# Kernel tuning notes

Hardware: AMD Instinct MI355X
Metric: run time of the kernel (lower is better)

Reference implementation:

```python
import jax, jax.numpy as jnp
import numpy as np
import math

N_NODES = 50000
N_EDGES = 800000
IN_DIM = 128
OUT_DIM = 64
TIME_DIM = 128


def setup_inputs() -> dict:
    key = jax.random.key(0)
    ks = jax.random.split(key, 9)
    return {
        "node_feats": jax.random.normal(ks[0], (N_NODES, IN_DIM), dtype=jnp.float32),
        "time_diff": jax.random.uniform(ks[1], (N_EDGES,), dtype=jnp.float32),
        "src": jax.random.randint(ks[2], (N_EDGES,), 0, N_NODES, dtype=jnp.int32),
        "dst": jax.random.randint(ks[3], (N_EDGES,), 0, N_NODES, dtype=jnp.int32),
        "W": jax.random.normal(ks[4], (OUT_DIM, IN_DIM), dtype=jnp.float32) * 0.05,
        "Wv": jax.random.normal(ks[5], (OUT_DIM, IN_DIM), dtype=jnp.float32) * 0.05,
        "omega": jax.random.normal(ks[6], (TIME_DIM // 2,), dtype=jnp.float32),
        "Wt": jax.random.normal(ks[7], (OUT_DIM, TIME_DIM), dtype=jnp.float32) * 0.05,
        "a": jax.random.normal(ks[8], (3 * OUT_DIM,), dtype=jnp.float32) * 0.05,
    }


def reference(node_feats, time_diff, src, dst, W, Wv, omega, Wt, a):
    N = node_feats.shape[0]
    d = W.shape[0]  # out_dim
    time_dim = 2 * omega.shape[0]

    # gather + linear projections per edge
    h_src = node_feats[src] @ W.T          # [E, d]
    h_dst = node_feats[dst] @ W.T          # [E, d]
    v_src = node_feats[src] @ Wv.T         # [E, d]

    # temporal encoding: interleaved sin/cos of t * omega, scaled by sqrt(1/dim)
    ang = time_diff[:, None] * omega[None, :]                       # [E, dim/2]
    pe = jnp.stack([jnp.sin(ang), jnp.cos(ang)], axis=-1)
    pe = pe.reshape(ang.shape[0], time_dim) * jnp.float32(math.sqrt(1.0 / time_dim))
    t_emb = pe @ Wt.T                                               # [E, d]

    # attn_fc(concat([h_src, h_dst, t_emb])) == split dot products (same math, no big concat)
    e = h_src @ a[:d] + h_dst @ a[d:2 * d] + t_emb @ a[2 * d:]      # [E]
    e = jnp.where(e > 0, e, 0.2 * e)  # LeakyReLU(0.2)

    # edge_softmax: softmax over incoming edges of each destination node
    m = jax.ops.segment_max(e, dst, num_segments=N)
    ex = jnp.exp(e - m[dst])
    den = jax.ops.segment_sum(ex, dst, num_segments=N)
    alpha = ex / den[dst]  # dropout is identity in eval mode

    # weighted message scatter-sum aggregation
    msg = v_src * alpha[:, None]                                    # [E, d]
    return jax.ops.segment_sum(msg, dst, num_segments=N)            # [N, d]
```

## Files before the change

kernel.cpp:

```cpp
#include <hip/hip_runtime.h>
#include <hip/hip_bf16.h>
#include <hip/hip_fp16.h>
#include <math.h>

#define IN_DIM   128
#define OUT_DIM  64
#define THALF    64
#define PE_SCALE 0.08838834764831845f
#define TBL      2048

typedef __attribute__((ext_vector_type(8))) short  short8;
typedef __attribute__((ext_vector_type(4))) float  f32x4;

__device__ inline unsigned short bf16_rne(float x) {
    unsigned u = __float_as_uint(x);
    return (unsigned short)((u + 0x7FFFu + ((u >> 16) & 1u)) >> 16);
}

__global__ __launch_bounds__(256) void k_params_pack(
    const float* __restrict__ W, const float* __restrict__ Wt,
    const float* __restrict__ a, const float* __restrict__ Wv,
    float* __restrict__ atv, unsigned short* __restrict__ Bp)
{
    __shared__ float saW1[IN_DIM], saW2[IN_DIM];
    int k = threadIdx.x;
    if (k < IN_DIM) {
        float x1 = 0.f, x2 = 0.f, x3 = 0.f;
        for (int j = 0; j < OUT_DIM; ++j) {
            float wj = W[j * IN_DIM + k];
            x1 += a[j] * wj;
            x2 += a[OUT_DIM + j] * wj;
            x3 += a[2 * OUT_DIM + j] * Wt[j * IN_DIM + k];
        }
        saW1[k] = x1; saW2[k] = x2; atv[k] = x3;
    }
    __syncthreads();
    for (int i = threadIdx.x; i < 5 * 4 * 64 * 8; i += 256) {
        int j    = i & 7;
        int lane = (i >> 3) & 63;
        int k0i  = (i >> 9) & 3;
        int t    = i >> 11;
        int kk = k0i * 32 + (lane >> 4) * 8 + j;
        int n  = lane & 15;
        float val;
        if (t < 4)      val = Wv[(t * 16 + n) * IN_DIM + kk];
        else            val = (n == 0) ? saW1[kk] : (n == 1) ? saW2[kk] : 0.f;
        Bp[i] = bf16_rne(val);
    }
}

__global__ __launch_bounds__(256) void k_gtab(
    const float* __restrict__ omega,
    const float* __restrict__ atv,
    float* __restrict__ gtab,
    int* __restrict__ cnt, int N)
{
    int idx = blockIdx.x * 256 + threadIdx.x;
    if (idx <= TBL) {
        float t = (float)idx * (1.0f / TBL);
        float acc = 0.f;
#pragma unroll
        for (int i = 0; i < THALF; ++i) {
            float sp, cp;
            __sincosf(t * omega[i], &sp, &cp);
            acc += sp * atv[2 * i] + cp * atv[2 * i + 1];
        }
        gtab[idx] = acc;
    }
    for (int i = idx; i < N; i += gridDim.x * 256) cnt[i] = 0;
}

__global__ __launch_bounds__(256) void k_node_mfma(
    const float* __restrict__ feats,
    const unsigned short* __restrict__ Bp,
    unsigned short* __restrict__ vb,
    float* __restrict__ s1,
    float* __restrict__ s2,
    int N)
{
    int gwave = (blockIdx.x * 256 + threadIdx.x) >> 6;
    int lane  = threadIdx.x & 63;
    int ntiles = (N + 15) >> 4;
    if (gwave >= ntiles) return;
    int row = lane & 15, quad = lane >> 4;
    int nodeA = gwave * 16 + row;
    int nodeL = nodeA < N ? nodeA : N - 1;

    const float* arow = feats + (size_t)nodeL * IN_DIM + quad * 8;
    short8 afrag[4];
#pragma unroll
    for (int k0i = 0; k0i < 4; ++k0i) {
        float4 fa = *(const float4*)(arow + k0i * 32);
        float4 fb = *(const float4*)(arow + k0i * 32 + 4);
        union { unsigned u[4]; short8 s; } cv;
        cv.u[0] = (__float_as_uint(fa.x) >> 16) | (__float_as_uint(fa.y) & 0xFFFF0000u);
        cv.u[1] = (__float_as_uint(fa.z) >> 16) | (__float_as_uint(fa.w) & 0xFFFF0000u);
        cv.u[2] = (__float_as_uint(fb.x) >> 16) | (__float_as_uint(fb.y) & 0xFFFF0000u);
        cv.u[3] = (__float_as_uint(fb.z) >> 16) | (__float_as_uint(fb.w) & 0xFFFF0000u);
        afrag[k0i] = cv.s;
    }

    const short8* B8 = (const short8*)Bp;
    f32x4 acc[5];
#pragma unroll
    for (int t = 0; t < 5; ++t) acc[t] = (f32x4){0.f, 0.f, 0.f, 0.f};
#pragma unroll
    for (int t = 0; t < 5; ++t) {
#pragma unroll
        for (int k0i = 0; k0i < 4; ++k0i)
            acc[t] = __builtin_amdgcn_mfma_f32_16x16x32_bf16(
                afrag[k0i], B8[(t * 4 + k0i) * 64 + lane], acc[t], 0, 0, 0);
    }

    int col = lane & 15;
    int baseNode = gwave * 16 + quad * 4;
#pragma unroll
    for (int r = 0; r < 4; ++r) {
        int nd = baseNode + r;
        if (nd < N) {
            unsigned short* vr = vb + (size_t)nd * OUT_DIM + col;
#pragma unroll
            for (int t = 0; t < 4; ++t) vr[t * 16] = bf16_rne(acc[t][r]);
            if (col == 0)      s1[nd] = acc[4][r];
            else if (col == 1) s2[nd] = acc[4][r];
        }
    }
}

__global__ __launch_bounds__(256) void k_logits_rank(
    const float* __restrict__ tdiff,
    const int* __restrict__ src,
    const int* __restrict__ dst,
    const float* __restrict__ gtab,
    const float* __restrict__ s1,
    const float* __restrict__ s2,
    int* __restrict__ cnt,
    int* __restrict__ rank,
    unsigned* __restrict__ payw,
    int E)
{
    int e = blockIdx.x * blockDim.x + threadIdx.x;
    if (e >= E) return;
    int s = src[e], d = dst[e];
    int rk = atomicAdd(cnt + d, 1);
    float a1 = s1[s];
    float a2 = s2[d];
    float t = tdiff[e];

    float x = t * (float)TBL;
    int i0 = (int)x;
    i0 = i0 < 0 ? 0 : (i0 > TBL - 1 ? TBL - 1 : i0);
    float fr = x - (float)i0;
    float g0 = gtab[i0], g1 = gtab[i0 + 1];
    float ev = a1 + a2 + PE_SCALE * (g0 + fr * (g1 - g0));
    ev = ev > 0.f ? ev : 0.2f * ev;

    rank[e] = rk;
    payw[e] = ((unsigned)s << 16) | (unsigned)__half_as_ushort(__float2half(ev));
}

__global__ __launch_bounds__(256) void k_scan1(const int* __restrict__ cnt,
                                               int* __restrict__ offs,
                                               int* __restrict__ bsum, int N)
{
    __shared__ int lds[256];
    int b = blockIdx.x, t = threadIdx.x;
    int base = b * 1024 + t * 4;
    int v0 = (base + 0 < N) ? cnt[base + 0] : 0;
    int v1 = (base + 1 < N) ? cnt[base + 1] : 0;
    int v2 = (base + 2 < N) ? cnt[base + 2] : 0;
    int v3 = (base + 3 < N) ? cnt[base + 3] : 0;
    int s = v0 + v1 + v2 + v3;
    lds[t] = s;
    __syncthreads();
    for (int off = 1; off < 256; off <<= 1) {
        int tmp = (t >= off) ? lds[t - off] : 0;
        __syncthreads();
        lds[t] += tmp;
        __syncthreads();
    }
    int ex = lds[t] - s;
    if (base + 0 < N) offs[base + 0] = ex;
    ex += v0;
    if (base + 1 < N) offs[base + 1] = ex;
    ex += v1;
    if (base + 2 < N) offs[base + 2] = ex;
    ex += v2;
    if (base + 3 < N) offs[base + 3] = ex;
    if (t == 255) bsum[b] = lds[255];
}

__global__ __launch_bounds__(256) void k_scan3(int* __restrict__ offs,
                                               const int* __restrict__ bsum,
                                               int N, int E)
{
    int i = blockIdx.x * 256 + threadIdx.x;
    if (i < N) {
        int c = i >> 10;
        int p = 0;
        for (int j = 0; j < c; ++j) p += bsum[j];
        offs[i] += p;
    }
    if (i == 0) offs[N] = E;
}

__global__ __launch_bounds__(256) void k_scatter(
    const int* __restrict__ dst,
    const int* __restrict__ rank,
    const unsigned* __restrict__ payw,
    const int* __restrict__ offs,
    unsigned* __restrict__ payload,
    int E)
{
    int e = blockIdx.x * blockDim.x + threadIdx.x;
    if (e >= E) return;
    payload[offs[dst[e]] + rank[e]] = payw[e];
}

__global__ __launch_bounds__(256) void k_aggregate(
    const int* __restrict__ offs,
    const unsigned* __restrict__ payload,
    const unsigned short* __restrict__ vb,
    float* __restrict__ out,
    int N)
{
    int wid  = (blockIdx.x * blockDim.x + threadIdx.x) >> 6;
    int lane = threadIdx.x & 63;
    if (wid >= N) return;
    int beg = offs[wid];
    int deg = offs[wid + 1] - beg;
    int g8 = lane >> 3, r = lane & 7;

    float acc[8];
#pragma unroll
    for (int i = 0; i < 8; ++i) acc[i] = 0.f;
    float den = 0.f;

    for (int base = 0; base < deg; base += 64) {
        int cl = deg - base; if (cl > 64) cl = 64;
        bool valid = lane < cl;
        unsigned pl = valid ? payload[beg + base + lane] : 0u;
        float ex = valid ? __expf(__half2float(__ushort_as_half((unsigned short)(pl & 0xFFFFu)))) : 0.f;
        int   sv = valid ? (int)(pl >> 16) : 0;

        float sum = ex;
#pragma unroll
        for (int off = 32; off; off >>= 1) sum += __shfl_xor(sum, off, 64);
        den += sum;

        int rounds = (cl + 15) >> 4;
        for (int j = 0; j < rounds; ++j) {
            int i0 = j * 16 + g8;
            int i1 = i0 + 8;
            float e0 = __shfl(ex, i0, 64);
            int   s0 = __shfl(sv, i0, 64);
            float e1 = __shfl(ex, i1, 64);
            int   s1v = __shfl(sv, i1, 64);
            uint4 w0 = *((const uint4*)(vb + (size_t)s0 * OUT_DIM) + r);
            uint4 w1 = *((const uint4*)(vb + (size_t)s1v * OUT_DIM) + r);
            acc[0] += e0 * __uint_as_float(w0.x << 16)        + e1 * __uint_as_float(w1.x << 16);
            acc[1] += e0 * __uint_as_float(w0.x & 0xFFFF0000u) + e1 * __uint_as_float(w1.x & 0xFFFF0000u);
            acc[2] += e0 * __uint_as_float(w0.y << 16)        + e1 * __uint_as_float(w1.y << 16);
            acc[3] += e0 * __uint_as_float(w0.y & 0xFFFF0000u) + e1 * __uint_as_float(w1.y & 0xFFFF0000u);
            acc[4] += e0 * __uint_as_float(w0.z << 16)        + e1 * __uint_as_float(w1.z << 16);
            acc[5] += e0 * __uint_as_float(w0.z & 0xFFFF0000u) + e1 * __uint_as_float(w1.z & 0xFFFF0000u);
            acc[6] += e0 * __uint_as_float(w0.w << 16)        + e1 * __uint_as_float(w1.w << 16);
            acc[7] += e0 * __uint_as_float(w0.w & 0xFFFF0000u) + e1 * __uint_as_float(w1.w & 0xFFFF0000u);
        }
    }

#pragma unroll
    for (int i = 0; i < 8; ++i) {
        acc[i] += __shfl_xor(acc[i], 8, 64);
        acc[i] += __shfl_xor(acc[i], 16, 64);
        acc[i] += __shfl_xor(acc[i], 32, 64);
    }

    if (g8 == 0) {
        float inv = (deg > 0) ? 1.f / den : 0.f;
        float* o = out + (size_t)wid * OUT_DIM + r * 8;
        *(float4*)(o)     = make_float4(acc[0] * inv, acc[1] * inv, acc[2] * inv, acc[3] * inv);
        *(float4*)(o + 4) = make_float4(acc[4] * inv, acc[5] * inv, acc[6] * inv, acc[7] * inv);
    }
}

extern "C" void kernel_launch(void* const* d_in, const int* in_sizes, int n_in,
                              void* d_out, int out_size, void* d_ws, size_t ws_size,
                              hipStream_t stream) {
    const float* feats = (const float*)d_in[0];
    const float* tdiff = (const float*)d_in[1];
    const int*   src   = (const int*)d_in[2];
    const int*   dst   = (const int*)d_in[3];
    const float* W     = (const float*)d_in[4];
    const float* Wv    = (const float*)d_in[5];
    const float* omega = (const float*)d_in[6];
    const float* Wt    = (const float*)d_in[7];
    const float* a     = (const float*)d_in[8];
    float* out = (float*)d_out;

    int N = in_sizes[0] / IN_DIM;
    int E = in_sizes[1];

    int offs_elems = ((N + 1 + 3) / 4) * 4;
    float* ws      = (float*)d_ws;
    unsigned short* vb = (unsigned short*)ws;
    float* s1      = ws + (size_t)N * 32;
    float* s2      = s1 + N;
    int*   rank    = (int*)(s2 + N);
    unsigned* payw = (unsigned*)(rank + E);
    unsigned* payload = payw + E;
    int*   cnt     = (int*)(payload + E);
    int*   offs    = cnt + N;
    int*   bsum    = offs + offs_elems;
    float* atv     = (float*)(bsum + 64);
    float* gtab    = atv + IN_DIM;
    unsigned short* Bp = (unsigned short*)(gtab + TBL + 1);

    int nb = (N + 1023) / 1024;
    int ntiles = (N + 15) / 16;

    k_params_pack<<<1, 256, 0, stream>>>(W, Wt, a, Wv, atv, Bp);
    k_gtab<<<64, 256, 0, stream>>>(omega, atv, gtab, cnt, N);
    k_node_mfma<<<(ntiles * 64 + 255) / 256, 256, 0, stream>>>(feats, Bp, vb, s1, s2, N);
    k_logits_rank<<<(E + 255) / 256, 256, 0, stream>>>(tdiff, src, dst, gtab, s1, s2, cnt, rank, payw, E);
    k_scan1<<<nb, 256, 0, stream>>>(cnt, offs, bsum, N);
    k_scan3<<<(N + 255) / 256, 256, 0, stream>>>(offs, bsum, N, E);
    k_scatter<<<(E + 255) / 256, 256, 0, stream>>>(dst, rank, payw, offs, payload, E);
    long long tot = (long long)N * OUT_DIM;
    k_aggregate<<<(int)((tot + 255) / 256), 256, 0, stream>>>(offs, payload, vb, out, N);
}
```

Measured before the change: 194.3 us.

## Fuse edge logits, counting scan and scatter into one cooperative kernel

Merges the edge logit/rank, two scan passes and the scatter into a single cooperative-groups kernel on 256 blocks, with grid syncs between phases. Per-edge rank, destination and payload stay in registers (up to 16 edges per thread), so the rank and payw global arrays and their round trip through memory go away. The cnt zeroing moves from k_gtab into the fused kernel. In exchange, the edge phase runs on only 65536 threads with serialised loops and the grid-wide syncs cost something. Correctness depends on E <= 16 x 65536 and on the cooperative launch succeeding.

```diff
diff --git a/kernel.cpp b/kernel.cpp
--- a/kernel.cpp
+++ b/kernel.cpp
@@ -1,13 +1,18 @@
 #include <hip/hip_runtime.h>
 #include <hip/hip_bf16.h>
 #include <hip/hip_fp16.h>
+#include <hip/hip_cooperative_groups.h>
 #include <math.h>
+
+namespace cg = cooperative_groups;
 
 #define IN_DIM   128
 #define OUT_DIM  64
 #define THALF    64
 #define PE_SCALE 0.08838834764831845f
 #define TBL      2048
+#define CB       256
+#define MAXE     16
 
 typedef __attribute__((ext_vector_type(8))) short  short8;
 typedef __attribute__((ext_vector_type(4))) float  f32x4;
@@ -52,22 +57,19 @@
 __global__ __launch_bounds__(256) void k_gtab(
     const float* __restrict__ omega,
     const float* __restrict__ atv,
-    float* __restrict__ gtab,
-    int* __restrict__ cnt, int N)
+    float* __restrict__ gtab)
 {
     int idx = blockIdx.x * 256 + threadIdx.x;
-    if (idx <= TBL) {
-        float t = (float)idx * (1.0f / TBL);
-        float acc = 0.f;
-#pragma unroll
-        for (int i = 0; i < THALF; ++i) {
-            float sp, cp;
-            __sincosf(t * omega[i], &sp, &cp);
-            acc += sp * atv[2 * i] + cp * atv[2 * i + 1];
-        }
-        gtab[idx] = acc;
-    }
-    for (int i = idx; i < N; i += gridDim.x * 256) cnt[i] = 0;
+    if (idx > TBL) return;
+    float t = (float)idx * (1.0f / TBL);
+    float acc = 0.f;
+#pragma unroll
+    for (int i = 0; i < THALF; ++i) {
+        float sp, cp;
+        __sincosf(t * omega[i], &sp, &cp);
+        acc += sp * atv[2 * i] + cp * atv[2 * i + 1];
+    }
+    gtab[idx] = acc;
 }
 
 __global__ __launch_bounds__(256) void k_node_mfma(
@@ -127,7 +129,7 @@
     }
 }
 
-__global__ __launch_bounds__(256) void k_logits_rank(
+__global__ __launch_bounds__(256) void k_edge_coop(
     const float* __restrict__ tdiff,
     const int* __restrict__ src,
     const int* __restrict__ dst,
@@ -135,86 +137,83 @@
     const float* __restrict__ s1,
     const float* __restrict__ s2,
     int* __restrict__ cnt,
-    int* __restrict__ rank,
-    unsigned* __restrict__ payw,
-    int E)
-{
-    int e = blockIdx.x * blockDim.x + threadIdx.x;
-    if (e >= E) return;
-    int s = src[e], d = dst[e];
-    int rk = atomicAdd(cnt + d, 1);
-    float a1 = s1[s];
-    float a2 = s2[d];
-    float t = tdiff[e];
-
-    float x = t * (float)TBL;
-    int i0 = (int)x;
-    i0 = i0 < 0 ? 0 : (i0 > TBL - 1 ? TBL - 1 : i0);
-    float fr = x - (float)i0;
-    float g0 = gtab[i0], g1 = gtab[i0 + 1];
-    float ev = a1 + a2 + PE_SCALE * (g0 + fr * (g1 - g0));
-    ev = ev > 0.f ? ev : 0.2f * ev;
-
-    rank[e] = rk;
-    payw[e] = ((unsigned)s << 16) | (unsigned)__half_as_ushort(__float2half(ev));
-}
-
-__global__ __launch_bounds__(256) void k_scan1(const int* __restrict__ cnt,
-                                               int* __restrict__ offs,
-                                               int* __restrict__ bsum, int N)
-{
+    int* __restrict__ offs,
+    int* __restrict__ bsum,
+    unsigned* __restrict__ payload,
+    int N, int E)
+{
+    cg::grid_group grid = cg::this_grid();
+    int tid = blockIdx.x * 256 + threadIdx.x;
+    const int T = CB * 256;
+
+    for (int i = tid; i < N; i += T) cnt[i] = 0;
+    grid.sync();
+
+    int      ed[MAXE];
+    int      rk[MAXE];
+    unsigned pw[MAXE];
+    int ne = 0;
+    for (int e = tid; e < E; e += T) {
+        int s = src[e], d = dst[e];
+        int r = atomicAdd(cnt + d, 1);
+        float a1 = s1[s];
+        float a2 = s2[d];
+        float t = tdiff[e];
+        float x = t * (float)TBL;
+        int i0 = (int)x;
+        i0 = i0 < 0 ? 0 : (i0 > TBL - 1 ? TBL - 1 : i0);
+        float fr = x - (float)i0;
+        float g0 = gtab[i0], g1 = gtab[i0 + 1];
+        float ev = a1 + a2 + PE_SCALE * (g0 + fr * (g1 - g0));
+        ev = ev > 0.f ? ev : 0.2f * ev;
+        ed[ne] = d;
+        rk[ne] = r;
+        pw[ne] = ((unsigned)s << 16) | (unsigned)__half_as_ushort(__float2half(ev));
+        ++ne;
+    }
+    grid.sync();
+
+    int nb = (N + 1023) >> 10;
     __shared__ int lds[256];
-    int b = blockIdx.x, t = threadIdx.x;
-    int base = b * 1024 + t * 4;
-    int v0 = (base + 0 < N) ? cnt[base + 0] : 0;
-    int v1 = (base + 1 < N) ? cnt[base + 1] : 0;
-    int v2 = (base + 2 < N) ? cnt[base + 2] : 0;
-    int v3 = (base + 3 < N) ? cnt[base + 3] : 0;
-    int s = v0 + v1 + v2 + v3;
-    lds[t] = s;
-    __syncthreads();
-    for (int off = 1; off < 256; off <<= 1) {
-        int tmp = (t >= off) ? lds[t - off] : 0;
+    if (blockIdx.x < nb) {
+        int b = blockIdx.x, t = threadIdx.x;
+        int base = b * 1024 + t * 4;
+        int v0 = (base + 0 < N) ? cnt[base + 0] : 0;
+        int v1 = (base + 1 < N) ? cnt[base + 1] : 0;
+        int v2 = (base + 2 < N) ? cnt[base + 2] : 0;
+        int v3 = (base + 3 < N) ? cnt[base + 3] : 0;
+        int s = v0 + v1 + v2 + v3;
+        lds[t] = s;
         __syncthreads();
-        lds[t] += tmp;
-        __syncthreads();
-    }
-    int ex = lds[t] - s;
-    if (base + 0 < N) offs[base + 0] = ex;
-    ex += v0;
-    if (base + 1 < N) offs[base + 1] = ex;
-    ex += v1;
-    if (base + 2 < N) offs[base + 2] = ex;
-    ex += v2;
-    if (base + 3 < N) offs[base + 3] = ex;
-    if (t == 255) bsum[b] = lds[255];
-}
-
-__global__ __launch_bounds__(256) void k_scan3(int* __restrict__ offs,
-                                               const int* __restrict__ bsum,
-                                               int N, int E)
-{
-    int i = blockIdx.x * 256 + threadIdx.x;
-    if (i < N) {
+        for (int off = 1; off < 256; off <<= 1) {
+            int tmp = (t >= off) ? lds[t - off] : 0;
+            __syncthreads();
+            lds[t] += tmp;
+            __syncthreads();
+        }
+        int ex = lds[t] - s;
+        if (base + 0 < N) offs[base + 0] = ex;
+        ex += v0;
+        if (base + 1 < N) offs[base + 1] = ex;
+        ex += v1;
+        if (base + 2 < N) offs[base + 2] = ex;
+        ex += v2;
+        if (base + 3 < N) offs[base + 3] = ex;
+        if (t == 255) bsum[b] = lds[255];
+    }
+    grid.sync();
+
+    for (int i = tid; i < N; i += T) {
         int c = i >> 10;
         int p = 0;
         for (int j = 0; j < c; ++j) p += bsum[j];
         offs[i] += p;
     }
-    if (i == 0) offs[N] = E;
-}
-
-__global__ __launch_bounds__(256) void k_scatter(
-    const int* __restrict__ dst,
-    const int* __restrict__ rank,
-    const unsigned* __restrict__ payw,
-    const int* __restrict__ offs,
-    unsigned* __restrict__ payload,
-    int E)
-{
-    int e = blockIdx.x * blockDim.x + threadIdx.x;
-    if (e >= E) return;
-    payload[offs[dst[e]] + rank[e]] = payw[e];
+    if (tid == 0) offs[N] = E;
+    grid.sync();
+
+    for (int k = 0; k < ne; ++k)
+        payload[offs[ed[k]] + rk[k]] = pw[k];
 }
 
 __global__ __launch_bounds__(256) void k_aggregate(
@@ -258,13 +257,13 @@
             int   s1v = __shfl(sv, i1, 64);
             uint4 w0 = *((const uint4*)(vb + (size_t)s0 * OUT_DIM) + r);
             uint4 w1 = *((const uint4*)(vb + (size_t)s1v * OUT_DIM) + r);
-            acc[0] += e0 * __uint_as_float(w0.x << 16)        + e1 * __uint_as_float(w1.x << 16);
+            acc[0] += e0 * __uint_as_float(w0.x << 16)         + e1 * __uint_as_float(w1.x << 16);
             acc[1] += e0 * __uint_as_float(w0.x & 0xFFFF0000u) + e1 * __uint_as_float(w1.x & 0xFFFF0000u);
-            acc[2] += e0 * __uint_as_float(w0.y << 16)        + e1 * __uint_as_float(w1.y << 16);
+            acc[2] += e0 * __uint_as_float(w0.y << 16)         + e1 * __uint_as_float(w1.y << 16);
             acc[3] += e0 * __uint_as_float(w0.y & 0xFFFF0000u) + e1 * __uint_as_float(w1.y & 0xFFFF0000u);
-            acc[4] += e0 * __uint_as_float(w0.z << 16)        + e1 * __uint_as_float(w1.z << 16);
+            acc[4] += e0 * __uint_as_float(w0.z << 16)         + e1 * __uint_as_float(w1.z << 16);
             acc[5] += e0 * __uint_as_float(w0.z & 0xFFFF0000u) + e1 * __uint_as_float(w1.z & 0xFFFF0000u);
-            acc[6] += e0 * __uint_as_float(w0.w << 16)        + e1 * __uint_as_float(w1.w << 16);
+            acc[6] += e0 * __uint_as_float(w0.w << 16)         + e1 * __uint_as_float(w1.w << 16);
             acc[7] += e0 * __uint_as_float(w0.w & 0xFFFF0000u) + e1 * __uint_as_float(w1.w & 0xFFFF0000u);
         }
     }
@@ -306,9 +305,7 @@
     unsigned short* vb = (unsigned short*)ws;
     float* s1      = ws + (size_t)N * 32;
     float* s2      = s1 + N;
-    int*   rank    = (int*)(s2 + N);
-    unsigned* payw = (unsigned*)(rank + E);
-    unsigned* payload = payw + E;
+    unsigned* payload = (unsigned*)(s2 + N);
     int*   cnt     = (int*)(payload + E);
     int*   offs    = cnt + N;
     int*   bsum    = offs + offs_elems;
@@ -316,16 +313,18 @@
     float* gtab    = atv + IN_DIM;
     unsigned short* Bp = (unsigned short*)(gtab + TBL + 1);
 
-    int nb = (N + 1023) / 1024;
     int ntiles = (N + 15) / 16;
 
     k_params_pack<<<1, 256, 0, stream>>>(W, Wt, a, Wv, atv, Bp);
-    k_gtab<<<64, 256, 0, stream>>>(omega, atv, gtab, cnt, N);
+    k_gtab<<<(TBL + 1 + 255) / 256, 256, 0, stream>>>(omega, atv, gtab);
     k_node_mfma<<<(ntiles * 64 + 255) / 256, 256, 0, stream>>>(feats, Bp, vb, s1, s2, N);
-    k_logits_rank<<<(E + 255) / 256, 256, 0, stream>>>(tdiff, src, dst, gtab, s1, s2, cnt, rank, payw, E);
-    k_scan1<<<nb, 256, 0, stream>>>(cnt, offs, bsum, N);
-    k_scan3<<<(N + 255) / 256, 256, 0, stream>>>(offs, bsum, N, E);
-    k_scatter<<<(E + 255) / 256, 256, 0, stream>>>(dst, rank, payw, offs, payload, E);
+
+    void* args[] = { (void*)&tdiff, (void*)&src, (void*)&dst, (void*)&gtab,
+                     (void*)&s1, (void*)&s2, (void*)&cnt, (void*)&offs,
+                     (void*)&bsum, (void*)&payload, (void*)&N, (void*)&E };
+    hipLaunchCooperativeKernel((void*)k_edge_coop, dim3(CB), dim3(256),
+                               args, 0, stream);
+
     long long tot = (long long)N * OUT_DIM;
     k_aggregate<<<(int)((tot + 255) / 256), 256, 0, stream>>>(offs, payload, vb, out, N);
 }
```

Measured after the change: 314.1 us. +61.7%, slower.
